# Kernel optimization log

Measured on AMD Instinct MI355X. Metric: run time of the kernel, lower is better.

Reference implementation:

```python
import jax, jax.numpy as jnp
import numpy as np

B, R, C1, C2, C3, K, NC = 512, 200, 32, 32, 512, 8, 2
RATIO = 0.5
K1 = int(np.ceil(RATIO * R))    # 100 nodes kept after pool1
K2 = int(np.ceil(RATIO * K1))   # 50 nodes kept after pool2
EDGE_P = 0.1
NEG = -1e9
BN_EPS = 1e-5
LEAK = 0.01


def setup_inputs() -> dict:
    key = jax.random.key(0)
    ks = jax.random.split(key, 12)

    def lin_w(k, o, i):
        return (jax.random.normal(k, (o, i)) / np.sqrt(i)).astype(jnp.float32)

    return {
        "x": jax.random.normal(ks[0], (B, R, R), dtype=jnp.float32),
        "adj": jax.random.uniform(ks[1], (B, R, R), dtype=jnp.float32),
        "roi": jnp.arange(R, dtype=jnp.int32),
        # conv1 ROI-conditioned weight net: Linear(R->K) -> ReLU -> Linear(K->R*C1)
        "W1a": lin_w(ks[2], K, R), "b1a": jnp.zeros((K,), jnp.float32),
        "W2a": lin_w(ks[3], R * C1, K), "b2a": jnp.zeros((R * C1,), jnp.float32),
        "bias1": jnp.zeros((C1,), jnp.float32),
        # conv2 ROI-conditioned weight net: Linear(R->K) -> ReLU -> Linear(K->C1*C2)
        "W1b": lin_w(ks[4], K, R), "b1b": jnp.zeros((K,), jnp.float32),
        "W2b": lin_w(ks[5], C1 * C2, K), "b2b": jnp.zeros((C1 * C2,), jnp.float32),
        "bias2": jnp.zeros((C2,), jnp.float32),
        # TopK pooling projection vectors
        "wp1": jax.random.normal(ks[6], (C1,), dtype=jnp.float32),
        "wp2": jax.random.normal(ks[7], (C2,), dtype=jnp.float32),
        # MLP head
        "Wm1": lin_w(ks[8], C2, (C1 + C2) * 2), "bm1": jnp.zeros((C2,), jnp.float32),
        "g1": jnp.ones((C2,), jnp.float32), "be1": jnp.zeros((C2,), jnp.float32),
        "Wm2": lin_w(ks[9], C3, C2), "bm2": jnp.zeros((C3,), jnp.float32),
        "g2": jnp.ones((C3,), jnp.float32), "be2": jnp.zeros((C3,), jnp.float32),
        "Ws": lin_w(ks[10], NC, C3), "bs": jnp.zeros((NC,), jnp.float32),
    }


def _nn_table(W1, b1, W2, b2, cin, cout):
    # nn applied to one-hot ROI vectors == table lookup; build the full [R, cin, cout] table once.
    t = jax.nn.relu(W1.T + b1) @ W2.T + b2  # [R, cin*cout]
    return t.reshape(R, cin, cout)


def _gconv(x, w_adj, mask, w_node, bias):
    # per-node ROI-conditioned transform, then edge-softmax weighted aggregation
    if w_node.ndim == 3:   # shared table indexed by arange -> [R,cin,cout]
        xt = jnp.einsum('bni,nio->bno', x, w_node)
    else:                   # gathered per graph -> [B,n,cin,cout]
        xt = jnp.einsum('bni,bnio->bno', x, w_node)
    n = x.shape[1]
    eye = jnp.eye(n, dtype=bool)
    # remove self loops, add self loop with weight 1, softmax over incoming edges
    logits = jnp.where(mask & ~eye, w_adj, NEG)
    logits = jnp.where(eye, 1.0, logits)
    att = jax.nn.softmax(logits, axis=-1)  # row i = incoming edges of node i
    return jnp.einsum('bij,bjo->bio', att, xt) + bias


def _topk_pool(h, w_adj, mask, roi, w, k):
    s = jax.nn.sigmoid(h @ w / jnp.linalg.norm(w))  # [B, n]
    vals, perm = jax.lax.top_k(s, k)
    xs = jnp.take_along_axis(h, perm[:, :, None], axis=1) * vals[:, :, None]
    b = jnp.arange(h.shape[0])[:, None, None]
    w_sub = w_adj[b, perm[:, :, None], perm[:, None, :]]
    m_sub = mask[b, perm[:, :, None], perm[:, None, :]]
    roi_sub = roi[perm] if roi.ndim == 1 else jnp.take_along_axis(roi, perm, axis=1)
    return xs, w_sub, m_sub, roi_sub, vals


def _augment(w_adj, mask):
    # add_self_loops(fill=1) -> spspmm(A, A) -> remove_self_loops, in dense-batched form
    n = w_adj.shape[1]
    eye = jnp.eye(n, dtype=bool)
    wd = jnp.where(mask & ~eye, w_adj, 0.0)
    wd = jnp.where(eye, 1.0, wd)
    a2 = jnp.einsum('bij,bjk->bik', wd, wd)
    m2 = (a2 != 0.0) & ~eye
    a2 = jnp.where(eye, 0.0, a2)
    return a2, m2


def _mlp_block(y, Wl, bl, g, be):
    y = y @ Wl.T + bl
    y = jnp.where(y > 0, y, LEAK * y)          # LeakyReLU(0.01)
    mu = jnp.mean(y, axis=0)
    var = jnp.var(y, axis=0)                    # training-mode BatchNorm1d
    return g * (y - mu) * jax.lax.rsqrt(var + BN_EPS) + be


def _forward(x, adj, roi, W1a, b1a, W2a, b2a, bias1, W1b, b1b, W2b, b2b, bias2,
             wp1, wp2, Wm1, bm1, g1, be1, Wm2, bm2, g2, be2, Ws, bs):
    mask0 = adj < EDGE_P
    wtab1 = _nn_table(W1a, b1a, W2a, b2a, R, C1)   # [R, R, C1]
    h1 = _gconv(x, adj, mask0, wtab1[roi], bias1)  # [B, R, C1]
    x1, w1, m1, roi1, vals1 = _topk_pool(h1, adj, mask0, roi, wp1, K1)
    a_aug, m_aug = _augment(w1, m1)                 # 2-hop augmented adjacency
    wtab2 = _nn_table(W1b, b1b, W2b, b2b, C1, C2)  # [R, C1, C2]
    h2 = _gconv(x1, a_aug, m_aug, wtab2[roi1], bias2)  # [B, K1, C2]
    x2, _, _, _, vals2 = _topk_pool(h2, a_aug, m_aug, roi1, wp2, K2)
    # readout: [gmp, gap] per level, concatenated -> (C1+C2)*2 = 128
    feat = jnp.concatenate([x1.max(1), x1.mean(1), x2.max(1), x2.mean(1)], axis=-1)
    y = _mlp_block(feat, Wm1, bm1, g1, be1)
    y = _mlp_block(y, Wm2, bm2, g2, be2)
    logp = jax.nn.log_softmax(y @ Ws.T + bs, axis=-1)
    return logp, jax.nn.sigmoid(vals1), jax.nn.sigmoid(vals2)


def reference(x, adj, roi, W1a, b1a, W2a, b2a, bias1, W1b, b1b, W2b, b2b, bias2,
              wp1, wp2, Wm1, bm1, g1, be1, Wm2, bm2, g2, be2, Ws, bs):
    logp, s1, s2 = _forward(x, adj, roi, W1a, b1a, W2a, b2a, bias1,
                            W1b, b1b, W2b, b2b, bias2, wp1, wp2,
                            Wm1, bm1, g1, be1, Wm2, bm2, g2, be2, Ws, bs)
    return (logp, wp1, wp2, s1, s2)
```

## Files before the change

kernel.cpp:

```cpp
#include <hip/hip_runtime.h>
#include <math.h>

#define NB 512
#define RR 200
#define KK1 100
#define KK2 50

__device__ __forceinline__ float sigm(float v) { return 1.0f / (1.0f + expf(-v)); }

__global__ void k_tab(const float* __restrict__ W1, const float* __restrict__ b1,
                      const float* __restrict__ W2, const float* __restrict__ b2,
                      float* __restrict__ tab, int OUT) {
  int n = blockIdx.x;
  __shared__ float h[8];
  if (threadIdx.x < 8) {
    float v = W1[threadIdx.x * RR + n] + b1[threadIdx.x];
    h[threadIdx.x] = v > 0.f ? v : 0.f;
  }
  __syncthreads();
  for (int j = threadIdx.x; j < OUT; j += 256) {
    float acc = b2[j];
#pragma unroll
    for (int k = 0; k < 8; k++) acc += h[k] * W2[j * 8 + k];
    tab[(size_t)n * OUT + j] = acc;
  }
}

__global__ void k_norm(const float* __restrict__ wp1, const float* __restrict__ wp2,
                       float* __restrict__ norms) {
  int t = threadIdx.x;
  float a = (t < 32) ? wp1[t] * wp1[t] : 0.f;
  float b = (t < 32) ? wp2[t] * wp2[t] : 0.f;
  for (int s = 32; s; s >>= 1) { a += __shfl_xor(a, s); b += __shfl_xor(b, s); }
  if (t == 0) { norms[0] = sqrtf(a); norms[1] = sqrtf(b); }
}

__global__ __launch_bounds__(256) void k_xt1(const float* __restrict__ x,
                                             const float* __restrict__ wtab1,
                                             float* __restrict__ xt1) {
  int n = blockIdx.x, t = threadIdx.x;
  __shared__ float wsm[6400];
  for (int idx = t; idx < 1600; idx += 256)
    *(float4*)&wsm[idx * 4] = *(const float4*)(wtab1 + (size_t)n * 6400 + idx * 4);
  __syncthreads();
  int w = t >> 6, lane = t & 63;
  int bg = lane >> 3, og = lane & 7;
  int b0 = blockIdx.y * 64 + w * 16 + bg * 2;
  const float* xp = x + (size_t)b0 * 40000 + (size_t)n * 200;
  float acc[2][4] = {};
  float4 A[2], Bf[2], N0[2] = {}, N1[2] = {};
#pragma unroll
  for (int r = 0; r < 2; r++) A[r] = *(const float4*)(xp + (size_t)r * 40000);
#pragma unroll
  for (int r = 0; r < 2; r++) Bf[r] = *(const float4*)(xp + (size_t)r * 40000 + 4);
  for (int g = 0; g < 50; g += 2) {
    int i = g * 4;
    if (g + 2 < 50) {
#pragma unroll
      for (int r = 0; r < 2; r++) N0[r] = *(const float4*)(xp + (size_t)r * 40000 + i + 8);
#pragma unroll
      for (int r = 0; r < 2; r++) N1[r] = *(const float4*)(xp + (size_t)r * 40000 + i + 12);
    }
#pragma unroll
    for (int k = 0; k < 4; k++) {
      float4 w4 = *(const float4*)&wsm[(i + k) * 32 + og * 4];
#pragma unroll
      for (int r = 0; r < 2; r++) {
        float xs = (&A[r].x)[k];
        acc[r][0] += xs * w4.x; acc[r][1] += xs * w4.y;
        acc[r][2] += xs * w4.z; acc[r][3] += xs * w4.w;
      }
    }
#pragma unroll
    for (int k = 0; k < 4; k++) {
      float4 w4 = *(const float4*)&wsm[(i + 4 + k) * 32 + og * 4];
#pragma unroll
      for (int r = 0; r < 2; r++) {
        float xs = (&Bf[r].x)[k];
        acc[r][0] += xs * w4.x; acc[r][1] += xs * w4.y;
        acc[r][2] += xs * w4.z; acc[r][3] += xs * w4.w;
      }
    }
#pragma unroll
    for (int r = 0; r < 2; r++) { A[r] = N0[r]; Bf[r] = N1[r]; }
  }
#pragma unroll
  for (int r = 0; r < 2; r++)
    *(float4*)(xt1 + (size_t)(b0 + r) * 6400 + (size_t)n * 32 + og * 4) =
        make_float4(acc[r][0], acc[r][1], acc[r][2], acc[r][3]);
}

__global__ __launch_bounds__(1024) void k_att1(const float* __restrict__ adj,
                                               const float* __restrict__ xt1,
                                               const float* __restrict__ bias1,
                                               const float* __restrict__ wp1,
                                               const float* __restrict__ norms,
                                               float* __restrict__ h1, float* __restrict__ sc1) {
  int t = threadIdx.x;
  __shared__ float pT[16][RR][4];
  int w = t >> 6, lane = t & 63;
  int og = lane & 7, jp = lane >> 3;
  float4 bias4 = *(const float4*)(bias1 + og * 4);
  float4 wp4 = *(const float4*)(wp1 + og * 4);
  float nrm = norms[0];
  int npass = (w < 2) ? 4 : 3;
  int total = 2 * npass;
  float av[4][4];
  {
    int b0 = blockIdx.x * 2;
    int r00 = w * 4;
    const float* abase = adj + (size_t)b0 * 40000 + (size_t)r00 * 200;
#pragma unroll
    for (int r = 0; r < 4; r++)
#pragma unroll
      for (int s2 = 0; s2 < 4; s2++) {
        int j = lane + 64 * s2;
        av[r][s2] = (j < RR) ? __builtin_nontemporal_load(abase + r * 200 + j) : 0.f;
      }
  }
  for (int idx = 0; idx < total; idx++) {
    int second = (idx >= npass) ? 1 : 0;
    int b = blockIdx.x * 2 + second;
    int pass = idx - second * npass;
    int r0 = pass * 64 + w * 4;
    const float* xtb = xt1 + (size_t)b * 6400 + og * 4;
    float p[4][4];
#pragma unroll
    for (int r = 0; r < 4; r++) {
      int i = r0 + r;
#pragma unroll
      for (int s2 = 0; s2 < 4; s2++) {
        int j = lane + 64 * s2;
        float e = 0.f;
        if (j < RR) {
          float a = av[r][s2];
          float lg = (j == i) ? 1.0f : ((a < 0.1f) ? a : -1e9f);
          e = __expf(lg - 1.0f);
        }
        p[r][s2] = e;
      }
    }
    if (idx + 1 < total) {
      int idx2 = idx + 1;
      int sec2 = (idx2 >= npass) ? 1 : 0;
      int b2 = blockIdx.x * 2 + sec2;
      int r02 = (idx2 - sec2 * npass) * 64 + w * 4;
      const float* abase = adj + (size_t)b2 * 40000 + (size_t)r02 * 200;
#pragma unroll
      for (int r = 0; r < 4; r++)
#pragma unroll
        for (int s2 = 0; s2 < 4; s2++) {
          int j = lane + 64 * s2;
          if (j < RR) av[r][s2] = __builtin_nontemporal_load(abase + r * 200 + j);
        }
    }
#pragma unroll
    for (int s2 = 0; s2 < 4; s2++) {
      int j = lane + 64 * s2;
      if (j < RR)
        *(float4*)&pT[w][j][0] = make_float4(p[0][s2], p[1][s2], p[2][s2], p[3][s2]);
    }
    float acc[4][4] = {};
    float ls[4] = {0.f, 0.f, 0.f, 0.f};
#pragma unroll 5
    for (int tj = 0; tj < 25; tj++) {
      int j = jp * 25 + tj;
      float4 pv = *(const float4*)&pT[w][j][0];
      float4 xv = *(const float4*)(xtb + j * 32);
      ls[0] += pv.x; ls[1] += pv.y; ls[2] += pv.z; ls[3] += pv.w;
      acc[0][0] += pv.x * xv.x; acc[0][1] += pv.x * xv.y; acc[0][2] += pv.x * xv.z; acc[0][3] += pv.x * xv.w;
      acc[1][0] += pv.y * xv.x; acc[1][1] += pv.y * xv.y; acc[1][2] += pv.y * xv.z; acc[1][3] += pv.y * xv.w;
      acc[2][0] += pv.z * xv.x; acc[2][1] += pv.z * xv.y; acc[2][2] += pv.z * xv.z; acc[2][3] += pv.z * xv.w;
      acc[3][0] += pv.w * xv.x; acc[3][1] += pv.w * xv.y; acc[3][2] += pv.w * xv.z; acc[3][3] += pv.w * xv.w;
    }
#pragma unroll
    for (int r = 0; r < 4; r++) {
      ls[r] += __shfl_xor(ls[r], 8); ls[r] += __shfl_xor(ls[r], 16); ls[r] += __shfl_xor(ls[r], 32);
#pragma unroll
      for (int c = 0; c < 4; c++) {
        float v = acc[r][c];
        v += __shfl_xor(v, 8); v += __shfl_xor(v, 16); v += __shfl_xor(v, 32);
        acc[r][c] = v;
      }
    }
#pragma unroll
    for (int r = 0; r < 4; r++) {
      if (jp == r) {
        float inv = 1.0f / ls[r];
        float4 h4 = make_float4(acc[r][0] * inv + bias4.x, acc[r][1] * inv + bias4.y,
                                acc[r][2] * inv + bias4.z, acc[r][3] * inv + bias4.w);
        *(float4*)(h1 + ((size_t)b * RR + r0 + r) * 32 + og * 4) = h4;
        float tt = h4.x * wp4.x + h4.y * wp4.y + h4.z * wp4.z + h4.w * wp4.w;
        tt += __shfl_xor(tt, 1); tt += __shfl_xor(tt, 2); tt += __shfl_xor(tt, 4);
        if (og == 0) sc1[b * RR + r0 + r] = sigm(tt / nrm);
      }
    }
  }
}

__global__ void k_top1(const float* __restrict__ sc1, int* __restrict__ perm1,
                       float* __restrict__ vals1, float* __restrict__ out_s1) {
  int b = blockIdx.x, t = threadIdx.x;
  __shared__ float s[RR];
  for (int i = t; i < RR; i += 256) s[i] = sc1[b * RR + i];
  __syncthreads();
  for (int i = t; i < RR; i += 256) {
    float si = s[i];
    int rank = 0;
    for (int j = 0; j < RR; j++) {
      float sj = s[j];
      rank += (sj > si) || (sj == si && j < i);
    }
    if (rank < KK1) {
      perm1[b * KK1 + rank] = i;
      vals1[b * KK1 + rank] = si;
      out_s1[b * KK1 + rank] = sigm(si);
    }
  }
}

__global__ __launch_bounds__(256) void k_stage2a(const float* __restrict__ h1,
                                                 const float* __restrict__ wtab2,
                                                 const int* __restrict__ perm1,
                                                 const float* __restrict__ vals1,
                                                 float* __restrict__ xt2,
                                                 float* __restrict__ feat) {
  int b = blockIdx.x, t = threadIdx.x;
  int kbase = blockIdx.y * 50;
  __shared__ float x1s[KK1 * 33];
  __shared__ int pk[KK1];
  __shared__ float vk[KK1];
  if (t < KK1) { pk[t] = perm1[b * KK1 + t]; vk[t] = vals1[b * KK1 + t]; }
  __syncthreads();
  for (int i = t; i < KK1 * 32; i += 256) {
    int k = i >> 5, o = i & 31;
    x1s[k * 33 + o] = h1[((size_t)b * RR + pk[k]) * 32 + o] * vk[k];
  }
  __syncthreads();
  if (blockIdx.y == 0 && t < 32) {
    float mx = -3e38f, sm = 0.f;
    for (int k = 0; k < KK1; k++) { float v = x1s[k * 33 + t]; mx = fmaxf(mx, v); sm += v; }
    feat[b * 128 + t] = mx;
    feat[b * 128 + 32 + t] = sm / 100.0f;
  }
  int w = t >> 6, lane = t & 63;
  int og = lane & 7, kq = lane >> 3;
#pragma unroll
  for (int pass = 0; pass < 2; pass++) {
    int kl = pass * 32 + w * 8 + kq;
    if (kl < 50) {
      int kg = kbase + kl;
      const float* W = wtab2 + (size_t)pk[kg] * 1024 + og * 4;
      float4 a4 = make_float4(0.f, 0.f, 0.f, 0.f);
#pragma unroll 8
      for (int ii = 0; ii < 32; ii++) {
        float4 w4 = *(const float4*)(W + ii * 32);
        float xs = x1s[kg * 33 + ii];
        a4.x += xs * w4.x; a4.y += xs * w4.y; a4.z += xs * w4.z; a4.w += xs * w4.w;
      }
      *(float4*)(xt2 + (size_t)b * 3200 + kg * 32 + og * 4) = a4;
    }
  }
}

__global__ __launch_bounds__(256) void k_wd(const float* __restrict__ adj,
                                            const int* __restrict__ perm1,
                                            float* __restrict__ wd) {
  int b = blockIdx.x, t = threadIdx.x;
  int g0 = blockIdx.y * 20;
  __shared__ float rowbuf[20][200];
  __shared__ int pk[KK1];
  if (t < KK1) pk[t] = perm1[b * KK1 + t];
  __syncthreads();
  for (int idx = t; idx < 4000; idx += 256) {
    int r = idx / 200, j = idx - r * 200;
    rowbuf[r][j] = adj[(size_t)b * 40000 + (size_t)pk[g0 + r] * 200 + j];
  }
  __syncthreads();
  for (int idx = t; idx < 2000; idx += 256) {
    int r = idx / 100, k2 = idx - r * 100;
    int k1 = g0 + r;
    float v;
    if (k1 == k2) v = 1.0f;
    else {
      float av = rowbuf[r][pk[k2]];
      v = (av < 0.1f) ? av : 0.0f;
    }
    wd[(size_t)b * (KK1 * KK1) + k1 * KK1 + k2] = v;
  }
}

__global__ __launch_bounds__(512) void k_stage2b(const float* __restrict__ wd,
                                                 const float* __restrict__ xt2,
                                                 const float* __restrict__ bias2,
                                                 const float* __restrict__ wp2,
                                                 const float* __restrict__ norms,
                                                 float* __restrict__ h2, float* __restrict__ sc2) {
  int b = blockIdx.x, t = threadIdx.x;
  __shared__ float wds[KK1][100];
  __shared__ float xts[KK1 * 32];
  __shared__ float pT[8][KK1][4];
  __shared__ int   nzidx[KK1][36];
  int w = t >> 6, lane = t & 63;
  unsigned long long ltmask = (1ull << lane) - 1ull;
  float bias_o = bias2[lane & 31];
  float wp_o = wp2[lane & 31];
  float nrm = norms[1];
  int k2a = lane;
  int k2b = lane + 64;
  bool vb = k2b < KK1;
  for (int i = t; i < KK1 * KK1; i += 512) ((float*)wds)[i] = wd[(size_t)b * (KK1 * KK1) + i];
  for (int idx = t; idx < 800; idx += 512)
    *(float4*)&xts[idx * 4] = *(const float4*)(xt2 + (size_t)b * 3200 + idx * 4);
  __syncthreads();
  for (int r = w; r < KK1; r += 8) {
    bool nz0 = (wds[r][lane] != 0.f);
    bool nz1 = (lane < KK1 - 64) && (wds[r][64 + lane] != 0.f);
    unsigned long long m0 = __ballot(nz0);
    unsigned long long m1 = __ballot(nz1);
    int c0 = __popcll(m0);
    int cnt = c0 + __popcll(m1);
    if (nz0) nzidx[r][__popcll(m0 & ltmask)] = lane;
    if (nz1) nzidx[r][c0 + __popcll(m1 & ltmask)] = 64 + lane;
    int pad = (4 - (cnt & 3)) & 3;
    if (lane < pad) nzidx[r][cnt + lane] = 0;
    if (lane == 0) nzidx[r][35] = cnt;
  }
  __syncthreads();
  for (int g = w; g < 25; g += 8) {
    int r0 = g * 4;
    float acc[4][2];
#pragma unroll
    for (int r = 0; r < 4; r++) {
      int k1 = r0 + r;
      int cnt = nzidx[k1][35];
      float s0 = 0.f, s1 = 0.f;
      for (int it = 0; it < cnt; it += 4) {
        int4 m4 = *(const int4*)&nzidx[k1][it];
        float a0 = wds[k1][m4.x];
        float a1 = (it + 1 < cnt) ? wds[k1][m4.y] : 0.f;
        float a2v = (it + 2 < cnt) ? wds[k1][m4.z] : 0.f;
        float a3 = (it + 3 < cnt) ? wds[k1][m4.w] : 0.f;
        s0 += a0 * wds[m4.x][k2a]; s1 += a0 * wds[m4.x][k2b];
        s0 += a1 * wds[m4.y][k2a]; s1 += a1 * wds[m4.y][k2b];
        s0 += a2v * wds[m4.z][k2a]; s1 += a2v * wds[m4.z][k2b];
        s0 += a3 * wds[m4.w][k2a]; s1 += a3 * wds[m4.w][k2b];
      }
      acc[r][0] = s0; acc[r][1] = s1;
    }
    float p0[4], p1[4], rs[4];
#pragma unroll
    for (int r = 0; r < 4; r++) {
      int k1 = r0 + r;
      float lv0 = (k1 == k2a) ? 1.0f : ((acc[r][0] != 0.0f) ? acc[r][0] : -1e9f);
      float lv1 = (k1 == k2b) ? 1.0f : ((acc[r][1] != 0.0f) ? acc[r][1] : -1e9f);
      float mx = vb ? fmaxf(lv0, lv1) : lv0;
      for (int s = 32; s; s >>= 1) mx = fmaxf(mx, __shfl_xor(mx, s));
      float e0 = expf(lv0 - mx);
      float e1 = vb ? expf(lv1 - mx) : 0.f;
      float ls = e0 + e1;
      for (int s = 32; s; s >>= 1) ls += __shfl_xor(ls, s);
      p0[r] = e0; p1[r] = e1; rs[r] = 1.0f / ls;
    }
    *(float4*)&pT[w][k2a][0] = make_float4(p0[0] * rs[0], p0[1] * rs[1], p0[2] * rs[2], p0[3] * rs[3]);
    if (vb) *(float4*)&pT[w][k2b][0] = make_float4(p1[0] * rs[0], p1[1] * rs[1], p1[2] * rs[2], p1[3] * rs[3]);
    int half = lane >> 5, o = lane & 31;
    float hv[4] = {0.f, 0.f, 0.f, 0.f};
    for (int jj = 0; jj < 50; jj++) {
      int j = half * 50 + jj;
      float4 pv = *(const float4*)&pT[w][j][0];
      float xv = xts[j * 32 + o];
      hv[0] += pv.x * xv; hv[1] += pv.y * xv; hv[2] += pv.z * xv; hv[3] += pv.w * xv;
    }
#pragma unroll
    for (int r = 0; r < 4; r++) hv[r] += __shfl_down(hv[r], 32);
    if (lane < 32) {
#pragma unroll
      for (int r = 0; r < 4; r++) {
        float h = hv[r] + bias_o;
        h2[((size_t)b * KK1 + (r0 + r)) * 32 + o] = h;
        float tt = h * wp_o;
        for (int s = 16; s; s >>= 1) tt += __shfl_xor(tt, s);
        if (lane == 0) sc2[b * KK1 + (r0 + r)] = sigm(tt / nrm);
      }
    }
  }
}

__global__ void k_feat2(const float* __restrict__ sc2, const float* __restrict__ h2,
                        float* __restrict__ out_s2, float* __restrict__ feat) {
  int b = blockIdx.x, t = threadIdx.x;
  __shared__ float s[KK1];
  __shared__ int p2[KK2];
  __shared__ float v2[KK2];
  for (int i = t; i < KK1; i += 256) s[i] = sc2[b * KK1 + i];
  __syncthreads();
  for (int i = t; i < KK1; i += 256) {
    float si = s[i];
    int rank = 0;
    for (int j = 0; j < KK1; j++) {
      float sj = s[j];
      rank += (sj > si) || (sj == si && j < i);
    }
    if (rank < KK2) {
      p2[rank] = i;
      v2[rank] = si;
      out_s2[b * KK2 + rank] = sigm(si);
    }
  }
  __syncthreads();
  if (t < 32) {
    float mx = -3e38f, sm = 0.f;
    for (int k = 0; k < KK2; k++) {
      float v = h2[((size_t)b * KK1 + p2[k]) * 32 + t] * v2[k];
      mx = fmaxf(mx, v);
      sm += v;
    }
    feat[b * 128 + 64 + t] = mx;
    feat[b * 128 + 96 + t] = sm / 50.0f;
  }
}

__global__ void k_mlp1(const float* __restrict__ feat, const float* __restrict__ Wm1,
                       const float* __restrict__ bm1, float* __restrict__ y1) {
  __shared__ float Wt[128 * 32];
  __shared__ float f[8][128];
  int t = threadIdx.x;
  for (int i = t; i < 4096; i += 256) { int c = i >> 7, d = i & 127; Wt[d * 32 + c] = Wm1[i]; }
  int b0 = blockIdx.x * 8;
  for (int i = t; i < 1024; i += 256) f[i >> 7][i & 127] = feat[b0 * 128 + i];
  __syncthreads();
  int bl = t >> 5, c = t & 31;
  float acc = bm1[c];
#pragma unroll 4
  for (int d = 0; d < 128; d++) acc += f[bl][d] * Wt[d * 32 + c];
  y1[(b0 + bl) * 32 + c] = acc > 0.f ? acc : 0.01f * acc;
}

__global__ void k_bn(const float* __restrict__ y, int C, float* __restrict__ stats) {
  int c = blockIdx.x, t = threadIdx.x;
  __shared__ float ys[512];
  __shared__ float red[8];
  ys[t] = y[(size_t)t * C + c];
  ys[t + 256] = y[(size_t)(t + 256) * C + c];
  __syncthreads();
  float s = ys[t] + ys[t + 256];
  for (int d = 32; d; d >>= 1) s += __shfl_xor(s, d);
  if ((t & 63) == 0) red[t >> 6] = s;
  __syncthreads();
  float mu = (red[0] + red[1] + red[2] + red[3]) * (1.0f / 512.0f);
  float d0 = ys[t] - mu, d1 = ys[t + 256] - mu;
  float v = d0 * d0 + d1 * d1;
  for (int d = 32; d; d >>= 1) v += __shfl_xor(v, d);
  if ((t & 63) == 0) red[4 + (t >> 6)] = v;
  __syncthreads();
  if (t == 0) {
    float var = (red[4] + red[5] + red[6] + red[7]) * (1.0f / 512.0f);
    stats[c] = mu;
    stats[C + c] = rsqrtf(var + 1e-5f);
  }
}

__global__ void k_mlp2(const float* __restrict__ y1, const float* __restrict__ st1,
                       const float* __restrict__ g1, const float* __restrict__ be1,
                       const float* __restrict__ Wm2, const float* __restrict__ bm2,
                       float* __restrict__ y2) {
  __shared__ float yn[32];
  int b = blockIdx.x, t = threadIdx.x;
  if (t < 32) {
    float v = y1[b * 32 + t];
    yn[t] = g1[t] * (v - st1[t]) * st1[32 + t] + be1[t];
  }
  __syncthreads();
  for (int c = t; c < 512; c += 256) {
    float acc = bm2[c];
#pragma unroll
    for (int k = 0; k < 32; k++) acc += yn[k] * Wm2[c * 32 + k];
    y2[(size_t)b * 512 + c] = acc > 0.f ? acc : 0.01f * acc;
  }
}

__global__ void k_final(const float* __restrict__ y2, const float* __restrict__ st2,
                        const float* __restrict__ g2, const float* __restrict__ be2,
                        const float* __restrict__ Ws, const float* __restrict__ bs,
                        float* __restrict__ out) {
  int w = threadIdx.x >> 6, lane = threadIdx.x & 63;
  int b = blockIdx.x * 4 + w;
  float z0 = 0.f, z1 = 0.f;
  for (int c = lane; c < 512; c += 64) {
    float v = g2[c] * (y2[(size_t)b * 512 + c] - st2[c]) * st2[512 + c] + be2[c];
    z0 += v * Ws[c];
    z1 += v * Ws[512 + c];
  }
  for (int s = 32; s; s >>= 1) { z0 += __shfl_xor(z0, s); z1 += __shfl_xor(z1, s); }
  if (lane == 0) {
    z0 += bs[0];
    z1 += bs[1];
    float m = fmaxf(z0, z1);
    float lse = m + logf(expf(z0 - m) + expf(z1 - m));
    out[b * 2] = z0 - lse;
    out[b * 2 + 1] = z1 - lse;
  }
}

__global__ void k_copy(const float* __restrict__ wp1, const float* __restrict__ wp2,
                       float* __restrict__ out) {
  int t = threadIdx.x;
  if (t < 32) out[1024 + t] = wp1[t];
  else if (t < 64) out[1056 + (t - 32)] = wp2[t - 32];
}

extern "C" void kernel_launch(void* const* d_in, const int* in_sizes, int n_in,
                              void* d_out, int out_size, void* d_ws, size_t ws_size,
                              hipStream_t stream) {
  const float* x    = (const float*)d_in[0];
  const float* adj  = (const float*)d_in[1];
  const float* W1a  = (const float*)d_in[3];
  const float* b1a  = (const float*)d_in[4];
  const float* W2a  = (const float*)d_in[5];
  const float* b2a  = (const float*)d_in[6];
  const float* bias1= (const float*)d_in[7];
  const float* W1b  = (const float*)d_in[8];
  const float* b1b  = (const float*)d_in[9];
  const float* W2b  = (const float*)d_in[10];
  const float* b2b  = (const float*)d_in[11];
  const float* bias2= (const float*)d_in[12];
  const float* wp1  = (const float*)d_in[13];
  const float* wp2  = (const float*)d_in[14];
  const float* Wm1  = (const float*)d_in[15];
  const float* bm1  = (const float*)d_in[16];
  const float* g1   = (const float*)d_in[17];
  const float* be1  = (const float*)d_in[18];
  const float* Wm2  = (const float*)d_in[19];
  const float* bm2  = (const float*)d_in[20];
  const float* g2   = (const float*)d_in[21];
  const float* be2  = (const float*)d_in[22];
  const float* Ws   = (const float*)d_in[23];
  const float* bs   = (const float*)d_in[24];
  float* out = (float*)d_out;

  float* ws = (float*)d_ws;
  float* WTAB1 = ws;
  float* WTAB2 = WTAB1 + 1280000;
  float* NORMS = WTAB2 + 204800;
  float* XT1   = NORMS + 16;
  float* H1    = XT1 + 3276800;
  float* SC1   = H1 + 3276800;
  float* VALS1 = SC1 + 102400;
  int*   PERM1 = (int*)(VALS1 + 51200);
  float* XT2   = (float*)(PERM1 + 51200);
  float* WD    = XT2 + 1638400;
  float* H2    = WD + 5120000;
  float* SC2   = H2 + 1638400;
  float* FEAT  = SC2 + 51200;
  float* Y1    = FEAT + 65536;
  float* ST1   = Y1 + 16384;
  float* Y2    = ST1 + 64;
  float* ST2   = Y2 + 262144;

  k_tab<<<200, 256, 0, stream>>>(W1a, b1a, W2a, b2a, WTAB1, 6400);
  k_tab<<<200, 256, 0, stream>>>(W1b, b1b, W2b, b2b, WTAB2, 1024);
  k_norm<<<1, 64, 0, stream>>>(wp1, wp2, NORMS);
  k_xt1<<<dim3(200, 8), 256, 0, stream>>>(x, WTAB1, XT1);
  k_att1<<<256, 1024, 0, stream>>>(adj, XT1, bias1, wp1, NORMS, H1, SC1);
  k_top1<<<512, 256, 0, stream>>>(SC1, PERM1, VALS1, out + 1088);
  k_stage2a<<<dim3(512, 2), 256, 0, stream>>>(H1, WTAB2, PERM1, VALS1, XT2, FEAT);
  k_wd<<<dim3(512, 5), 256, 0, stream>>>(adj, PERM1, WD);
  k_stage2b<<<512, 512, 0, stream>>>(WD, XT2, bias2, wp2, NORMS, H2, SC2);
  k_feat2<<<512, 256, 0, stream>>>(SC2, H2, out + 52288, FEAT);
  k_mlp1<<<64, 256, 0, stream>>>(FEAT, Wm1, bm1, Y1);
  k_bn<<<32, 256, 0, stream>>>(Y1, 32, ST1);
  k_mlp2<<<512, 256, 0, stream>>>(Y1, ST1, g1, be1, Wm2, bm2, Y2);
  k_bn<<<512, 256, 0, stream>>>(Y2, 512, ST2);
  k_final<<<128, 256, 0, stream>>>(Y2, ST2, g2, be2, Ws, bs, out);
  k_copy<<<1, 64, 0, stream>>>(wp1, wp2, out);
}
```

Before: 216.4 us.

## Compact sparse attention neighbors via ballot and widen xt1 per-thread batch tile

In k_att1, each row's nonzero edge-softmax weights (about 10% of entries) are packed with ballot/popcount into a per-wave shared list of (weight, index) pairs. The aggregation then loops only over those kept neighbors instead of all 200 columns. The softmax sum is now taken with a full-wave shuffle reduction. Separately, k_xt1 drops to 128 threads, with each thread computing 4 batch rows instead of 2 to reuse more shared weights per load, at the cost of more registers and fewer threads per block. The sparse loop adds load imbalance across lanes and data-dependent gather addresses.

```diff
diff --git a/kernel.cpp b/kernel.cpp
--- a/kernel.cpp
+++ b/kernel.cpp
@@ -35,37 +35,36 @@
   if (t == 0) { norms[0] = sqrtf(a); norms[1] = sqrtf(b); }
 }
 
-__global__ __launch_bounds__(256) void k_xt1(const float* __restrict__ x,
+__global__ __launch_bounds__(128) void k_xt1(const float* __restrict__ x,
                                              const float* __restrict__ wtab1,
                                              float* __restrict__ xt1) {
   int n = blockIdx.x, t = threadIdx.x;
   __shared__ float wsm[6400];
-  for (int idx = t; idx < 1600; idx += 256)
+  for (int idx = t; idx < 1600; idx += 128)
     *(float4*)&wsm[idx * 4] = *(const float4*)(wtab1 + (size_t)n * 6400 + idx * 4);
   __syncthreads();
-  int w = t >> 6, lane = t & 63;
-  int bg = lane >> 3, og = lane & 7;
-  int b0 = blockIdx.y * 64 + w * 16 + bg * 2;
+  int bg = t >> 3, og = t & 7;
+  int b0 = blockIdx.y * 64 + bg * 4;
   const float* xp = x + (size_t)b0 * 40000 + (size_t)n * 200;
-  float acc[2][4] = {};
-  float4 A[2], Bf[2], N0[2] = {}, N1[2] = {};
-#pragma unroll
-  for (int r = 0; r < 2; r++) A[r] = *(const float4*)(xp + (size_t)r * 40000);
-#pragma unroll
-  for (int r = 0; r < 2; r++) Bf[r] = *(const float4*)(xp + (size_t)r * 40000 + 4);
+  float acc[4][4] = {};
+  float4 A[4], Bf[4], N0[4] = {}, N1[4] = {};
+#pragma unroll
+  for (int r = 0; r < 4; r++) A[r] = *(const float4*)(xp + (size_t)r * 40000);
+#pragma unroll
+  for (int r = 0; r < 4; r++) Bf[r] = *(const float4*)(xp + (size_t)r * 40000 + 4);
   for (int g = 0; g < 50; g += 2) {
     int i = g * 4;
     if (g + 2 < 50) {
 #pragma unroll
-      for (int r = 0; r < 2; r++) N0[r] = *(const float4*)(xp + (size_t)r * 40000 + i + 8);
-#pragma unroll
-      for (int r = 0; r < 2; r++) N1[r] = *(const float4*)(xp + (size_t)r * 40000 + i + 12);
+      for (int r = 0; r < 4; r++) N0[r] = *(const float4*)(xp + (size_t)r * 40000 + i + 8);
+#pragma unroll
+      for (int r = 0; r < 4; r++) N1[r] = *(const float4*)(xp + (size_t)r * 40000 + i + 12);
     }
 #pragma unroll
     for (int k = 0; k < 4; k++) {
       float4 w4 = *(const float4*)&wsm[(i + k) * 32 + og * 4];
 #pragma unroll
-      for (int r = 0; r < 2; r++) {
+      for (int r = 0; r < 4; r++) {
         float xs = (&A[r].x)[k];
         acc[r][0] += xs * w4.x; acc[r][1] += xs * w4.y;
         acc[r][2] += xs * w4.z; acc[r][3] += xs * w4.w;
@@ -75,17 +74,17 @@
     for (int k = 0; k < 4; k++) {
       float4 w4 = *(const float4*)&wsm[(i + 4 + k) * 32 + og * 4];
 #pragma unroll
-      for (int r = 0; r < 2; r++) {
+      for (int r = 0; r < 4; r++) {
         float xs = (&Bf[r].x)[k];
         acc[r][0] += xs * w4.x; acc[r][1] += xs * w4.y;
         acc[r][2] += xs * w4.z; acc[r][3] += xs * w4.w;
       }
     }
 #pragma unroll
-    for (int r = 0; r < 2; r++) { A[r] = N0[r]; Bf[r] = N1[r]; }
-  }
-#pragma unroll
-  for (int r = 0; r < 2; r++)
+    for (int r = 0; r < 4; r++) { A[r] = N0[r]; Bf[r] = N1[r]; }
+  }
+#pragma unroll
+  for (int r = 0; r < 4; r++)
     *(float4*)(xt1 + (size_t)(b0 + r) * 6400 + (size_t)n * 32 + og * 4) =
         make_float4(acc[r][0], acc[r][1], acc[r][2], acc[r][3]);
 }
@@ -97,12 +96,13 @@
                                                const float* __restrict__ norms,
                                                float* __restrict__ h1, float* __restrict__ sc1) {
   int t = threadIdx.x;
-  __shared__ float pT[16][RR][4];
+  __shared__ float2 pvj[16][4][56];
   int w = t >> 6, lane = t & 63;
   int og = lane & 7, jp = lane >> 3;
   float4 bias4 = *(const float4*)(bias1 + og * 4);
   float4 wp4 = *(const float4*)(wp1 + og * 4);
   float nrm = norms[0];
+  unsigned long long ltmask = (1ull << lane) - 1ull;
   int npass = (w < 2) ? 4 : 3;
   int total = 2 * npass;
   float av[4][4];
@@ -115,7 +115,7 @@
 #pragma unroll
       for (int s2 = 0; s2 < 4; s2++) {
         int j = lane + 64 * s2;
-        av[r][s2] = (j < RR) ? __builtin_nontemporal_load(abase + r * 200 + j) : 0.f;
+        av[r][s2] = (j < RR) ? __builtin_nontemporal_load(abase + r * 200 + j) : 1.0f;
       }
   }
   for (int idx = 0; idx < total; idx++) {
@@ -123,22 +123,33 @@
     int b = blockIdx.x * 2 + second;
     int pass = idx - second * npass;
     int r0 = pass * 64 + w * 4;
-    const float* xtb = xt1 + (size_t)b * 6400 + og * 4;
-    float p[4][4];
+    float ls[4];
+    int cnt[4];
 #pragma unroll
     for (int r = 0; r < 4; r++) {
       int i = r0 + r;
+      float e[4];
+      bool nz[4];
 #pragma unroll
       for (int s2 = 0; s2 < 4; s2++) {
         int j = lane + 64 * s2;
-        float e = 0.f;
-        if (j < RR) {
-          float a = av[r][s2];
-          float lg = (j == i) ? 1.0f : ((a < 0.1f) ? a : -1e9f);
-          e = __expf(lg - 1.0f);
-        }
-        p[r][s2] = e;
-      }
+        float a = av[r][s2];
+        bool keep = (j < RR) && ((j == i) || (a < 0.1f));
+        float lg = (j == i) ? 1.0f : a;
+        e[s2] = keep ? __expf(lg - 1.0f) : 0.f;
+        nz[s2] = keep;
+      }
+      float lsum = e[0] + e[1] + e[2] + e[3];
+      int base = 0;
+#pragma unroll
+      for (int s2 = 0; s2 < 4; s2++) {
+        unsigned long long m = __ballot(nz[s2]);
+        if (nz[s2]) pvj[w][r][base + __popcll(m & ltmask)] = make_float2(e[s2], (float)(lane + 64 * s2));
+        base += __popcll(m);
+      }
+      cnt[r] = base;
+      for (int s = 32; s; s >>= 1) lsum += __shfl_xor(lsum, s);
+      ls[r] = lsum;
     }
     if (idx + 1 < total) {
       int idx2 = idx + 1;
@@ -154,28 +165,20 @@
           if (j < RR) av[r][s2] = __builtin_nontemporal_load(abase + r * 200 + j);
         }
     }
-#pragma unroll
-    for (int s2 = 0; s2 < 4; s2++) {
-      int j = lane + 64 * s2;
-      if (j < RR)
-        *(float4*)&pT[w][j][0] = make_float4(p[0][s2], p[1][s2], p[2][s2], p[3][s2]);
-    }
+    const float* xtb = xt1 + (size_t)b * 6400 + og * 4;
     float acc[4][4] = {};
-    float ls[4] = {0.f, 0.f, 0.f, 0.f};
-#pragma unroll 5
-    for (int tj = 0; tj < 25; tj++) {
-      int j = jp * 25 + tj;
-      float4 pv = *(const float4*)&pT[w][j][0];
-      float4 xv = *(const float4*)(xtb + j * 32);
-      ls[0] += pv.x; ls[1] += pv.y; ls[2] += pv.z; ls[3] += pv.w;
-      acc[0][0] += pv.x * xv.x; acc[0][1] += pv.x * xv.y; acc[0][2] += pv.x * xv.z; acc[0][3] += pv.x * xv.w;
-      acc[1][0] += pv.y * xv.x; acc[1][1] += pv.y * xv.y; acc[1][2] += pv.y * xv.z; acc[1][3] += pv.y * xv.w;
-      acc[2][0] += pv.z * xv.x; acc[2][1] += pv.z * xv.y; acc[2][2] += pv.z * xv.z; acc[2][3] += pv.z * xv.w;
-      acc[3][0] += pv.w * xv.x; acc[3][1] += pv.w * xv.y; acc[3][2] += pv.w * xv.z; acc[3][3] += pv.w * xv.w;
-    }
 #pragma unroll
     for (int r = 0; r < 4; r++) {
-      ls[r] += __shfl_xor(ls[r], 8); ls[r] += __shfl_xor(ls[r], 16); ls[r] += __shfl_xor(ls[r], 32);
+      for (int q = jp; q < cnt[r]; q += 8) {
+        float2 pe = pvj[w][r][q];
+        int jj = (int)pe.y;
+        float4 xv = *(const float4*)(xtb + jj * 32);
+        acc[r][0] += pe.x * xv.x; acc[r][1] += pe.x * xv.y;
+        acc[r][2] += pe.x * xv.z; acc[r][3] += pe.x * xv.w;
+      }
+    }
+#pragma unroll
+    for (int r = 0; r < 4; r++) {
 #pragma unroll
       for (int c = 0; c < 4; c++) {
         float v = acc[r][c];
@@ -561,7 +564,7 @@
   k_tab<<<200, 256, 0, stream>>>(W1a, b1a, W2a, b2a, WTAB1, 6400);
   k_tab<<<200, 256, 0, stream>>>(W1b, b1b, W2b, b2b, WTAB2, 1024);
   k_norm<<<1, 64, 0, stream>>>(wp1, wp2, NORMS);
-  k_xt1<<<dim3(200, 8), 256, 0, stream>>>(x, WTAB1, XT1);
+  k_xt1<<<dim3(200, 8), 128, 0, stream>>>(x, WTAB1, XT1);
   k_att1<<<256, 1024, 0, stream>>>(adj, XT1, bias1, wp1, NORMS, H1, SC1);
   k_top1<<<512, 256, 0, stream>>>(SC1, PERM1, VALS1, out + 1088);
   k_stage2a<<<dim3(512, 2), 256, 0, stream>>>(H1, WTAB2, PERM1, VALS1, XT2, FEAT);
```

New measurement: 224.1 us. 3.5% more time.
